# Kernel tuning notes

Measured on AMD Instinct MI355X. Metric: run time of the kernel, lower is better.

## Reference

```python
import jax, jax.numpy as jnp
import numpy as np

N, K, D = 8192, 512, 4096

def setup_inputs() -> dict:
    key = jax.random.key(0)
    k1, k2, k3 = jax.random.split(key, 3)
    features = jax.random.normal(k1, (N, K), dtype=jnp.float32)
    w = jax.random.normal(k2, (D, N), dtype=jnp.float32)
    E = jax.random.normal(k3, (K, D), dtype=jnp.float32) / np.sqrt(K)  # embed_matrix (k x d)
    b = jnp.zeros((D,), dtype=jnp.float32)  # bias initialized to zeros in the module
    return {"features": features, "w": w, "E": E, "b": b}

def reference(features, w, E, b):
    # Linear: y = features @ E + b  -> (N, D)   (torch weight is E.mT, so x @ W.T == x @ E)
    y = features @ E + b
    # diag(y @ w): equivalent to row-wise dot products, same math without the NxN matmul
    return jnp.einsum("nd,dn->n", y, w)
```

## Files before the change

### kernel.cpp

```cpp
#include <hip/hip_runtime.h>

#define N_DIM 8192
#define K_DIM 512
#define D_DIM 4096

typedef __bf16 bf16x8 __attribute__((ext_vector_type(8)));
typedef float  f32x16 __attribute__((ext_vector_type(16)));
typedef unsigned short u16x8 __attribute__((ext_vector_type(8)));

__device__ __forceinline__ unsigned short f2bf(float f) {
    union { float f; unsigned int u; } v; v.f = f;
    unsigned int r = v.u + 0x7FFF + ((v.u >> 16) & 1);
    return (unsigned short)(r >> 16);
}

__global__ __launch_bounds__(256) void transpose_E(const float* __restrict__ E,
                                                   unsigned short* __restrict__ ET) {
    __shared__ float tile[64][65];
    const int d0 = blockIdx.x * 64;
    const int k0 = blockIdx.y * 64;
    const int tid = threadIdx.x;
    const int r  = tid / 16;
    const int c4 = (tid % 16) * 4;
#pragma unroll
    for (int p = 0; p < 4; ++p) {
        int k = p * 16 + r;
        float4 v = *reinterpret_cast<const float4*>(E + (size_t)(k0 + k) * D_DIM + d0 + c4);
        tile[k][c4 + 0] = v.x; tile[k][c4 + 1] = v.y;
        tile[k][c4 + 2] = v.z; tile[k][c4 + 3] = v.w;
    }
    __syncthreads();
#pragma unroll
    for (int p = 0; p < 4; ++p) {
        int d = p * 16 + r;
        ushort4 o;
        o.x = f2bf(tile[c4 + 0][d]);
        o.y = f2bf(tile[c4 + 1][d]);
        o.z = f2bf(tile[c4 + 2][d]);
        o.w = f2bf(tile[c4 + 3][d]);
        *reinterpret_cast<ushort4*>(ET + (size_t)(d0 + d) * K_DIM + k0 + c4) = o;
    }
}

__global__ __launch_bounds__(256) void convert_F(const float* __restrict__ F,
                                                 unsigned short* __restrict__ FB,
                                                 float* __restrict__ out) {
    if (blockIdx.x < 8) {
        float4 z = {0.f, 0.f, 0.f, 0.f};
        *reinterpret_cast<float4*>(out + (blockIdx.x * 256 + threadIdx.x) * 4) = z;
    }
    const int idx8 = (blockIdx.x * 256 + threadIdx.x) * 8;
    float4 a = *reinterpret_cast<const float4*>(F + idx8);
    float4 b = *reinterpret_cast<const float4*>(F + idx8 + 4);
    u16x8 o;
    o[0] = f2bf(a.x); o[1] = f2bf(a.y); o[2] = f2bf(a.z); o[3] = f2bf(a.w);
    o[4] = f2bf(b.x); o[5] = f2bf(b.y); o[6] = f2bf(b.z); o[7] = f2bf(b.w);
    *reinterpret_cast<u16x8*>(FB + idx8) = o;
}

__global__ __launch_bounds__(256, 2) void gemm_fused(const unsigned short* __restrict__ FB,
                                                     const float* __restrict__ W,
                                                     const unsigned short* __restrict__ ET,
                                                     const float* __restrict__ B,
                                                     float* __restrict__ out) {
    __shared__ unsigned short Ash[2 * 128 * 32];
    __shared__ unsigned short Bsh[2 * 128 * 32];

    const int tid  = threadIdx.x;
    const int wave = tid >> 6;
    const int lane = tid & 63;
    const int wy   = wave >> 1;
    const int wx   = wave & 1;
    const int l31  = lane & 31;
    const int half = lane >> 5;

    const int f   = blockIdx.x + ((int)gridDim.x) * blockIdx.y;
    const int xcd = f & 7;
    const int s   = f >> 3;
    const int ntile = (xcd & 3) * 16 + (s & 15);
    const int dtile = (xcd >> 2) * 16 + (s >> 4);
    const int n0 = ntile * 128;
    const int d0 = dtile * 128;

    f32x16 acc[2][2] = {};
    float  wreg[2][16][2];

    const float* Wt = W + (size_t)(d0 + wy * 64 + 4 * half) * N_DIM + n0 + wx * 64 + l31;

    const int srow   = lane >> 2;
    const int schunk = (((lane & 3) ^ ((srow >> 1) & 3)) * 8);

#pragma unroll
    for (int kt = 0; kt < K_DIM / 64; ++kt) {
        const int kb = kt * 64;
#pragma unroll
        for (int p = 0; p < 2; ++p) {
#pragma unroll
            for (int jj = 0; jj < 2; ++jj) {
                const int j = wave * 2 + jj;
                const unsigned short* ga =
                    ET + (size_t)(d0 + j * 16 + srow) * K_DIM + kb + p * 32 + schunk;
                __builtin_amdgcn_global_load_lds(
                    (const __attribute__((address_space(1))) void*)ga,
                    (__attribute__((address_space(3))) void*)(Ash + p * 4096 + j * 512),
                    16, 0, 0);
                const unsigned short* gb =
                    FB + (size_t)(n0 + j * 16 + srow) * K_DIM + kb + p * 32 + schunk;
                __builtin_amdgcn_global_load_lds(
                    (const __attribute__((address_space(1))) void*)gb,
                    (__attribute__((address_space(3))) void*)(Bsh + p * 4096 + j * 512),
                    16, 0, 0);
            }
        }
        asm volatile("" ::: "memory");

#pragma unroll
        for (int rr = 0; rr < 2; ++rr) {
            const int reg   = kt * 2 + rr;
            const int droff = (reg & 3) + 8 * (reg >> 2);
#pragma unroll
            for (int mi = 0; mi < 2; ++mi)
#pragma unroll
                for (int ni = 0; ni < 2; ++ni)
                    wreg[mi][reg][ni] = __builtin_nontemporal_load(
                        Wt + (size_t)(mi * 32 + droff) * N_DIM + ni * 32);
        }
        asm volatile("" ::: "memory");

        asm volatile("s_waitcnt vmcnt(8)" ::: "memory");
        __builtin_amdgcn_sched_barrier(0);
        __builtin_amdgcn_s_barrier();
        __builtin_amdgcn_sched_barrier(0);

#pragma unroll
        for (int ks = 0; ks < 4; ++ks) {
            const int p = ks >> 1;
            const int c = (ks & 1) * 2 + half;
            bf16x8 af[2], bfr[2];
#pragma unroll
            for (int mi = 0; mi < 2; ++mi) {
                const int R = wy * 64 + mi * 32 + l31;
                const int slot = c ^ ((R >> 1) & 3);
                af[mi] = *reinterpret_cast<const bf16x8*>(
                    Ash + p * 4096 + R * 32 + slot * 8);
            }
#pragma unroll
            for (int ni = 0; ni < 2; ++ni) {
                const int R = wx * 64 + ni * 32 + l31;
                const int slot = c ^ ((R >> 1) & 3);
                bfr[ni] = *reinterpret_cast<const bf16x8*>(
                    Bsh + p * 4096 + R * 32 + slot * 8);
            }
#pragma unroll
            for (int mi = 0; mi < 2; ++mi)
#pragma unroll
                for (int ni = 0; ni < 2; ++ni)
                    acc[mi][ni] = __builtin_amdgcn_mfma_f32_32x32x16_bf16(
                        af[mi], bfr[ni], acc[mi][ni], 0, 0, 0);
        }

        __builtin_amdgcn_sched_barrier(0);
        __builtin_amdgcn_s_barrier();
        __builtin_amdgcn_sched_barrier(0);
    }

    const int nb = n0 + wx * 64;
    float part0 = 0.f, part1 = 0.f;
#pragma unroll
    for (int mi = 0; mi < 2; ++mi) {
        const int dbase = d0 + wy * 64 + mi * 32 + 4 * half;
#pragma unroll
        for (int reg = 0; reg < 16; ++reg) {
            const int dd = dbase + (reg & 3) + 8 * (reg >> 2);
            const float bd = B[dd];
            part0 += (acc[mi][0][reg] + bd) * wreg[mi][reg][0];
            part1 += (acc[mi][1][reg] + bd) * wreg[mi][reg][1];
        }
    }
    part0 += __shfl_xor(part0, 32);
    part1 += __shfl_xor(part1, 32);
    if (lane < 32) {
        atomicAdd(out + nb + l31, part0);
        atomicAdd(out + nb + 32 + l31, part1);
    }
}

extern "C" void kernel_launch(void* const* d_in, const int* in_sizes, int n_in,
                              void* d_out, int out_size, void* d_ws, size_t ws_size,
                              hipStream_t stream) {
    const float* F = (const float*)d_in[0];
    const float* W = (const float*)d_in[1];
    const float* E = (const float*)d_in[2];
    const float* B = (const float*)d_in[3];
    float* out = (float*)d_out;

    unsigned short* ET = (unsigned short*)d_ws;
    unsigned short* FB = (unsigned short*)((char*)d_ws + (size_t)D_DIM * K_DIM * 2);

    transpose_E<<<dim3(D_DIM / 64, K_DIM / 64), 256, 0, stream>>>(E, ET);
    convert_F<<<dim3(N_DIM * K_DIM / (256 * 8)), 256, 0, stream>>>(F, FB, out);
    gemm_fused<<<dim3(N_DIM / 128, D_DIM / 128), 256, 0, stream>>>(FB, W, ET, B, out);
}
```

Baseline: 237.7 us.

## Double-buffer LDS tiles and defer W loads to the epilogue

Doubles the shared-memory A/B tiles so the next K-slice's global-to-LDS copies are issued before computing on the current slice, overlapping loads with MFMA work. The W values, previously prefetched into 64 registers across the K loop, are now loaded directly in the epilogue. This removes one barrier per iteration and frees registers. In exchange, LDS use doubles (64 KB per block at 2 blocks/CU), and the epilogue W loads are no longer hidden behind compute, which exposes their memory latency.

After: 242.1 us. No clear change (+1.9%).

```diff
diff --git a/kernel.cpp b/kernel.cpp
--- a/kernel.cpp
+++ b/kernel.cpp
@@ -63,8 +63,8 @@
                                                      const unsigned short* __restrict__ ET,
                                                      const float* __restrict__ B,
                                                      float* __restrict__ out) {
-    __shared__ unsigned short Ash[2 * 128 * 32];
-    __shared__ unsigned short Bsh[2 * 128 * 32];
+    __shared__ unsigned short Ash[2 * 2 * 128 * 32];
+    __shared__ unsigned short Bsh[2 * 2 * 128 * 32];
 
     const int tid  = threadIdx.x;
     const int wave = tid >> 6;
@@ -83,54 +83,44 @@
     const int d0 = dtile * 128;
 
     f32x16 acc[2][2] = {};
-    float  wreg[2][16][2];
-
-    const float* Wt = W + (size_t)(d0 + wy * 64 + 4 * half) * N_DIM + n0 + wx * 64 + l31;
 
     const int srow   = lane >> 2;
     const int schunk = (((lane & 3) ^ ((srow >> 1) & 3)) * 8);
 
+#define STAGE(BUF, KT)                                                              \
+    {                                                                               \
+        const int kb_ = (KT) * 64;                                                  \
+        _Pragma("unroll")                                                           \
+        for (int p = 0; p < 2; ++p) {                                               \
+            _Pragma("unroll")                                                       \
+            for (int jj = 0; jj < 2; ++jj) {                                        \
+                const int j = wave * 2 + jj;                                        \
+                const unsigned short* ga =                                          \
+                    ET + (size_t)(d0 + j * 16 + srow) * K_DIM + kb_ + p * 32 + schunk; \
+                __builtin_amdgcn_global_load_lds(                                   \
+                    (const __attribute__((address_space(1))) void*)ga,              \
+                    (__attribute__((address_space(3))) void*)(Ash + (BUF) * 8192 + p * 4096 + j * 512), \
+                    16, 0, 0);                                                      \
+                const unsigned short* gb =                                          \
+                    FB + (size_t)(n0 + j * 16 + srow) * K_DIM + kb_ + p * 32 + schunk; \
+                __builtin_amdgcn_global_load_lds(                                   \
+                    (const __attribute__((address_space(1))) void*)gb,              \
+                    (__attribute__((address_space(3))) void*)(Bsh + (BUF) * 8192 + p * 4096 + j * 512), \
+                    16, 0, 0);                                                      \
+            }                                                                       \
+        }                                                                           \
+    }
+
+    STAGE(0, 0);
+    asm volatile("s_waitcnt vmcnt(0)" ::: "memory");
+    __builtin_amdgcn_sched_barrier(0);
+    __builtin_amdgcn_s_barrier();
+    __builtin_amdgcn_sched_barrier(0);
+
 #pragma unroll
     for (int kt = 0; kt < K_DIM / 64; ++kt) {
-        const int kb = kt * 64;
-#pragma unroll
-        for (int p = 0; p < 2; ++p) {
-#pragma unroll
-            for (int jj = 0; jj < 2; ++jj) {
-                const int j = wave * 2 + jj;
-                const unsigned short* ga =
-                    ET + (size_t)(d0 + j * 16 + srow) * K_DIM + kb + p * 32 + schunk;
-                __builtin_amdgcn_global_load_lds(
-                    (const __attribute__((address_space(1))) void*)ga,
-                    (__attribute__((address_space(3))) void*)(Ash + p * 4096 + j * 512),
-                    16, 0, 0);
-                const unsigned short* gb =
-                    FB + (size_t)(n0 + j * 16 + srow) * K_DIM + kb + p * 32 + schunk;
-                __builtin_amdgcn_global_load_lds(
-                    (const __attribute__((address_space(1))) void*)gb,
-                    (__attribute__((address_space(3))) void*)(Bsh + p * 4096 + j * 512),
-                    16, 0, 0);
-            }
-        }
-        asm volatile("" ::: "memory");
-
-#pragma unroll
-        for (int rr = 0; rr < 2; ++rr) {
-            const int reg   = kt * 2 + rr;
-            const int droff = (reg & 3) + 8 * (reg >> 2);
-#pragma unroll
-            for (int mi = 0; mi < 2; ++mi)
-#pragma unroll
-                for (int ni = 0; ni < 2; ++ni)
-                    wreg[mi][reg][ni] = __builtin_nontemporal_load(
-                        Wt + (size_t)(mi * 32 + droff) * N_DIM + ni * 32);
-        }
-        asm volatile("" ::: "memory");
-
-        asm volatile("s_waitcnt vmcnt(8)" ::: "memory");
-        __builtin_amdgcn_sched_barrier(0);
-        __builtin_amdgcn_s_barrier();
-        __builtin_amdgcn_sched_barrier(0);
+        const int cur = kt & 1;
+        if (kt < K_DIM / 64 - 1) STAGE(cur ^ 1, kt + 1);
 
 #pragma unroll
         for (int ks = 0; ks < 4; ++ks) {
@@ -142,14 +132,14 @@
                 const int R = wy * 64 + mi * 32 + l31;
                 const int slot = c ^ ((R >> 1) & 3);
                 af[mi] = *reinterpret_cast<const bf16x8*>(
-                    Ash + p * 4096 + R * 32 + slot * 8);
+                    Ash + cur * 8192 + p * 4096 + R * 32 + slot * 8);
             }
 #pragma unroll
             for (int ni = 0; ni < 2; ++ni) {
                 const int R = wx * 64 + ni * 32 + l31;
                 const int slot = c ^ ((R >> 1) & 3);
                 bfr[ni] = *reinterpret_cast<const bf16x8*>(
-                    Bsh + p * 4096 + R * 32 + slot * 8);
+                    Bsh + cur * 8192 + p * 4096 + R * 32 + slot * 8);
             }
 #pragma unroll
             for (int mi = 0; mi < 2; ++mi)
@@ -160,9 +150,11 @@
         }
 
         __builtin_amdgcn_sched_barrier(0);
+        asm volatile("s_waitcnt vmcnt(0)" ::: "memory");
         __builtin_amdgcn_s_barrier();
         __builtin_amdgcn_sched_barrier(0);
     }
+#undef STAGE
 
     const int nb = n0 + wx * 64;
     float part0 = 0.f, part1 = 0.f;
@@ -173,8 +165,9 @@
         for (int reg = 0; reg < 16; ++reg) {
             const int dd = dbase + (reg & 3) + 8 * (reg >> 2);
             const float bd = B[dd];
-            part0 += (acc[mi][0][reg] + bd) * wreg[mi][reg][0];
-            part1 += (acc[mi][1][reg] + bd) * wreg[mi][reg][1];
+            const float* wr = W + (size_t)dd * N_DIM + nb;
+            part0 += (acc[mi][0][reg] + bd) * __builtin_nontemporal_load(wr + l31);
+            part1 += (acc[mi][1][reg] + bd) * __builtin_nontemporal_load(wr + 32 + l31);
         }
     }
     part0 += __shfl_xor(part0, 32);
```

## Enlarge fused GEMM tile to 256x256 with 512 threads, load W in epilogue

Applied to the files above, without the earlier changes.

Doubles the block tile in both N and D to 256x256, using 8 waves per block with a 1D swizzled grid, so each block reuses its staged E and features tiles across more outputs. The W prefetch that was interleaved with the K loop is removed. W is now read with nontemporal loads directly in the epilogue, and the wait becomes vmcnt(0). This cuts redundant global traffic for the bf16 operands. In exchange, the dominant W stream is no longer overlapped with the MFMA work, and LDS use rises to 64KB per block, which limits occupancy.

Result: slower. 780.2 us (+228.3%).

```diff
diff --git a/kernel.cpp b/kernel.cpp
--- a/kernel.cpp
+++ b/kernel.cpp
@@ -58,34 +58,31 @@
     *reinterpret_cast<u16x8*>(FB + idx8) = o;
 }
 
-__global__ __launch_bounds__(256, 2) void gemm_fused(const unsigned short* __restrict__ FB,
+__global__ __launch_bounds__(512, 4) void gemm_fused(const unsigned short* __restrict__ FB,
                                                      const float* __restrict__ W,
                                                      const unsigned short* __restrict__ ET,
                                                      const float* __restrict__ B,
                                                      float* __restrict__ out) {
-    __shared__ unsigned short Ash[2 * 128 * 32];
-    __shared__ unsigned short Bsh[2 * 128 * 32];
+    __shared__ unsigned short Ash[2 * 256 * 32];
+    __shared__ unsigned short Bsh[2 * 256 * 32];
 
     const int tid  = threadIdx.x;
     const int wave = tid >> 6;
     const int lane = tid & 63;
-    const int wy   = wave >> 1;
-    const int wx   = wave & 1;
+    const int wd   = wave >> 2;
+    const int wn   = wave & 3;
     const int l31  = lane & 31;
     const int half = lane >> 5;
 
-    const int f   = blockIdx.x + ((int)gridDim.x) * blockIdx.y;
+    const int f   = blockIdx.x;
     const int xcd = f & 7;
     const int s   = f >> 3;
-    const int ntile = (xcd & 3) * 16 + (s & 15);
-    const int dtile = (xcd >> 2) * 16 + (s >> 4);
-    const int n0 = ntile * 128;
-    const int d0 = dtile * 128;
+    const int ntile = xcd * 4 + (s & 3);
+    const int dtile = s >> 2;
+    const int n0 = ntile * 256;
+    const int d0 = dtile * 256;
 
-    f32x16 acc[2][2] = {};
-    float  wreg[2][16][2];
-
-    const float* Wt = W + (size_t)(d0 + wy * 64 + 4 * half) * N_DIM + n0 + wx * 64 + l31;
+    f32x16 acc[4][2] = {};
 
     const int srow   = lane >> 2;
     const int schunk = (((lane & 3) ^ ((srow >> 1) & 3)) * 8);
@@ -102,32 +99,17 @@
                     ET + (size_t)(d0 + j * 16 + srow) * K_DIM + kb + p * 32 + schunk;
                 __builtin_amdgcn_global_load_lds(
                     (const __attribute__((address_space(1))) void*)ga,
-                    (__attribute__((address_space(3))) void*)(Ash + p * 4096 + j * 512),
+                    (__attribute__((address_space(3))) void*)(Ash + p * 8192 + j * 512),
                     16, 0, 0);
                 const unsigned short* gb =
                     FB + (size_t)(n0 + j * 16 + srow) * K_DIM + kb + p * 32 + schunk;
                 __builtin_amdgcn_global_load_lds(
                     (const __attribute__((address_space(1))) void*)gb,
-                    (__attribute__((address_space(3))) void*)(Bsh + p * 4096 + j * 512),
+                    (__attribute__((address_space(3))) void*)(Bsh + p * 8192 + j * 512),
                     16, 0, 0);
             }
         }
-        asm volatile("" ::: "memory");
-
-#pragma unroll
-        for (int rr = 0; rr < 2; ++rr) {
-            const int reg   = kt * 2 + rr;
-            const int droff = (reg & 3) + 8 * (reg >> 2);
-#pragma unroll
-            for (int mi = 0; mi < 2; ++mi)
-#pragma unroll
-                for (int ni = 0; ni < 2; ++ni)
-                    wreg[mi][reg][ni] = __builtin_nontemporal_load(
-                        Wt + (size_t)(mi * 32 + droff) * N_DIM + ni * 32);
-        }
-        asm volatile("" ::: "memory");
-
-        asm volatile("s_waitcnt vmcnt(8)" ::: "memory");
+        asm volatile("s_waitcnt vmcnt(0)" ::: "memory");
         __builtin_amdgcn_sched_barrier(0);
         __builtin_amdgcn_s_barrier();
         __builtin_amdgcn_sched_barrier(0);
@@ -136,23 +118,23 @@
         for (int ks = 0; ks < 4; ++ks) {
             const int p = ks >> 1;
             const int c = (ks & 1) * 2 + half;
-            bf16x8 af[2], bfr[2];
+            bf16x8 af[4], bfr[2];
 #pragma unroll
-            for (int mi = 0; mi < 2; ++mi) {
-                const int R = wy * 64 + mi * 32 + l31;
+            for (int mi = 0; mi < 4; ++mi) {
+                const int R = wd * 128 + mi * 32 + l31;
                 const int slot = c ^ ((R >> 1) & 3);
                 af[mi] = *reinterpret_cast<const bf16x8*>(
-                    Ash + p * 4096 + R * 32 + slot * 8);
+                    Ash + p * 8192 + R * 32 + slot * 8);
             }
 #pragma unroll
             for (int ni = 0; ni < 2; ++ni) {
-                const int R = wx * 64 + ni * 32 + l31;
+                const int R = wn * 64 + ni * 32 + l31;
                 const int slot = c ^ ((R >> 1) & 3);
                 bfr[ni] = *reinterpret_cast<const bf16x8*>(
-                    Bsh + p * 4096 + R * 32 + slot * 8);
+                    Bsh + p * 8192 + R * 32 + slot * 8);
             }
 #pragma unroll
-            for (int mi = 0; mi < 2; ++mi)
+            for (int mi = 0; mi < 4; ++mi)
 #pragma unroll
                 for (int ni = 0; ni < 2; ++ni)
                     acc[mi][ni] = __builtin_amdgcn_mfma_f32_32x32x16_bf16(
@@ -164,17 +146,18 @@
         __builtin_amdgcn_sched_barrier(0);
     }
 
-    const int nb = n0 + wx * 64;
+    const int nb = n0 + wn * 64;
     float part0 = 0.f, part1 = 0.f;
 #pragma unroll
-    for (int mi = 0; mi < 2; ++mi) {
-        const int dbase = d0 + wy * 64 + mi * 32 + 4 * half;
+    for (int mi = 0; mi < 4; ++mi) {
+        const int dbase = d0 + wd * 128 + mi * 32 + 4 * half;
 #pragma unroll
         for (int reg = 0; reg < 16; ++reg) {
             const int dd = dbase + (reg & 3) + 8 * (reg >> 2);
             const float bd = B[dd];
-            part0 += (acc[mi][0][reg] + bd) * wreg[mi][reg][0];
-            part1 += (acc[mi][1][reg] + bd) * wreg[mi][reg][1];
+            const float* wr = W + (size_t)dd * N_DIM + nb;
+            part0 += (acc[mi][0][reg] + bd) * __builtin_nontemporal_load(wr + l31);
+            part1 += (acc[mi][1][reg] + bd) * __builtin_nontemporal_load(wr + 32 + l31);
         }
     }
     part0 += __shfl_xor(part0, 32);
@@ -199,5 +182,5 @@
 
     transpose_E<<<dim3(D_DIM / 64, K_DIM / 64), 256, 0, stream>>>(E, ET);
     convert_F<<<dim3(N_DIM * K_DIM / (256 * 8)), 256, 0, stream>>>(F, FB, out);
-    gemm_fused<<<dim3(N_DIM / 128, D_DIM / 128), 256, 0, stream>>>(FB, W, ET, B, out);
+    gemm_fused<<<dim3((N_DIM / 256) * (D_DIM / 256)), 512, 0, stream>>>(FB, W, ET, B, out);
 }
```
